# Optimization experiments

Measured on AMD Instinct MI355X. Metric: run time of the kernel, lower is better.

## Reference

```python
import jax, jax.numpy as jnp
import numpy as np

HEADS = 4
DIM_HEAD = 32
SCALE = DIM_HEAD ** -0.5


def setup_inputs() -> dict:
    key = jax.random.key(0)
    k1, k2, k3 = jax.random.split(key, 3)
    dim, hidden = 256, HEADS * DIM_HEAD
    x = jax.random.normal(k1, (4, dim, 64, 64), dtype=jnp.float32)
    w_qkv = jax.random.normal(k2, (hidden * 3, dim), dtype=jnp.float32) * (dim ** -0.5)
    w_out = jax.random.normal(k3, (dim, hidden), dtype=jnp.float32) * (hidden ** -0.5)
    b_out = jnp.zeros((dim,), dtype=jnp.float32)
    return {"x": x, "w_qkv": w_qkv, "w_out": w_out, "b_out": b_out}


def reference(x, w_qkv, w_out, b_out):
    b, c, h, w = x.shape
    # 1x1 conv (no bias) == channel matmul
    qkv = jnp.einsum('bchw,oc->bohw', x, w_qkv)           # [b, 3*hidden, h, w]
    q, k, v = jnp.split(qkv, 3, axis=1)
    def to_heads(t):
        # [b, heads*d, h, w] -> [b, heads, h*w, d]
        return t.reshape(b, HEADS, DIM_HEAD, h * w).transpose(0, 1, 3, 2)
    q, k, v = to_heads(q) * SCALE, to_heads(k), to_heads(v)
    sim = jnp.einsum('bhid,bhjd->bhij', q, k)             # [b, heads, hw, hw]
    attn = jax.nn.softmax(sim, axis=-1)
    out = jnp.einsum('bhij,bhjd->bhid', attn, v)          # [b, heads, hw, d]
    out = out.transpose(0, 1, 3, 2).reshape(b, HEADS * DIM_HEAD, h, w)
    # output 1x1 conv with bias
    return jnp.einsum('bchw,oc->bohw', out, w_out) + b_out[None, :, None, None]
```

## Files before the change

### kernel.cpp

```cpp
#include <hip/hip_runtime.h>
#include <hip/hip_fp16.h>

#define HEADS 4
#define DH    32
#define HW    4096
#define CIN   256
#define HID   128
#define KSPLIT 2
#define KHALF (HW / KSPLIT)

using half8   = __attribute__((ext_vector_type(8))) _Float16;
using half4   = __attribute__((ext_vector_type(4))) _Float16;
using half2v  = __attribute__((ext_vector_type(2))) _Float16;
using floatx4 = __attribute__((ext_vector_type(4))) float;

#define SHIFT2 4.328085122666891f
#define WQSCALE 0.25508275947f

static __device__ __forceinline__ half2v pk2(float a, float b) {
  return __builtin_bit_cast(half2v, __builtin_amdgcn_cvt_pkrtz(a, b));
}

__global__ __launch_bounds__(256) void qkv_fused(
    const float* __restrict__ w, const float* __restrict__ x,
    _Float16* __restrict__ Qw, _Float16* __restrict__ Kw,
    _Float16* __restrict__ Vtw)
{
  __shared__ float t[64][65];
  __shared__ _Float16 As[64][72];
  __shared__ _Float16 Bs[64][72];
  const int mt = blockIdx.x, nt = blockIdx.y;
  const int b = nt >> 6, p0 = (nt & 63) * 64;
  const int tid = threadIdx.x;
  const int wv = tid >> 6, lane = tid & 63, lm = lane & 15, quad = lane >> 4;
  const float wscale = (mt < 2) ? WQSCALE : 1.0f;

  const float* Ag = w + (size_t)(mt * 64) * CIN;
  const float* xb = x + (size_t)b * CIN * HW + p0;

  floatx4 acc[4] = {{0,0,0,0},{0,0,0,0},{0,0,0,0},{0,0,0,0}};

  for (int kq = 0; kq < 4; ++kq) {
    __syncthreads();
    #pragma unroll
    for (int i = 0; i < 4; ++i) {
      int ci = tid + i * 256;
      int cc = ci >> 4, p4 = (ci & 15) * 4;
      *(float4*)&t[cc][p4] =
          *(const float4*)(xb + (size_t)(kq * 64 + cc) * HW + p4);
    }
    #pragma unroll
    for (int i = 0; i < 2; ++i) {
      int ci = tid + i * 256;
      int r = ci >> 3, c8 = (ci & 7) * 8;
      const float* src = Ag + (size_t)r * CIN + kq * 64 + c8;
      float4 u0 = *(const float4*)(src);
      float4 u1 = *(const float4*)(src + 4);
      half8 h = {(_Float16)(u0.x * wscale), (_Float16)(u0.y * wscale),
                 (_Float16)(u0.z * wscale), (_Float16)(u0.w * wscale),
                 (_Float16)(u1.x * wscale), (_Float16)(u1.y * wscale),
                 (_Float16)(u1.z * wscale), (_Float16)(u1.w * wscale)};
      *(half8*)&As[r][c8] = h;
    }
    __syncthreads();
    #pragma unroll
    for (int i = 0; i < 2; ++i) {
      int idx = tid + i * 256;
      int p = idx >> 3, c0 = (idx & 7) * 8;
      half8 v;
      #pragma unroll
      for (int k = 0; k < 8; ++k) v[k] = (_Float16)t[c0 + k][p];
      *(half8*)&Bs[p][c0] = v;
    }
    __syncthreads();
    #pragma unroll
    for (int ks = 0; ks < 2; ++ks) {
      half8 a = *(const half8*)&As[wv * 16 + lm][ks * 32 + quad * 8];
      #pragma unroll
      for (int ns = 0; ns < 4; ++ns) {
        half8 bf = *(const half8*)&Bs[ns * 16 + lm][ks * 32 + quad * 8];
        acc[ns] = __builtin_amdgcn_mfma_f32_16x16x32_f16(a, bf, acc[ns], 0, 0, 0);
      }
    }
  }

  const int sec = mt >> 1;
  const int o_base = (mt & 1) * 64 + wv * 16 + quad * 4;
  const int hh = o_base >> 5, dd = o_base & 31;
  const int bh = b * HEADS + hh;
  if (sec < 2) {
    _Float16* dst = (sec == 0) ? Qw : Kw;
    #pragma unroll
    for (int ns = 0; ns < 4; ++ns) {
      int p = p0 + ns * 16 + lm;
      half4 v = {(_Float16)acc[ns][0], (_Float16)acc[ns][1],
                 (_Float16)acc[ns][2], (_Float16)acc[ns][3]};
      *(half4*)(dst + ((size_t)bh * HW + p) * DH + dd) = v;
    }
  } else {
    #pragma unroll
    for (int ns = 0; ns < 4; ++ns) {
      int p = p0 + ns * 16 + lm;
      #pragma unroll
      for (int r = 0; r < 4; ++r)
        Vtw[((size_t)bh * DH + dd + r) * HW + p] = (_Float16)acc[ns][r];
    }
  }
}

__global__ __launch_bounds__(256) void attn(
    const _Float16* __restrict__ Qw, const _Float16* __restrict__ Kw,
    const _Float16* __restrict__ Vtw, float* __restrict__ Op,
    float* __restrict__ lp)
{
  __shared__ _Float16 ks[2][64][40];
  __shared__ _Float16 vt[2][32][74];

  const int bh = blockIdx.y, qt = blockIdx.x, z = blockIdx.z;
  const int tid = threadIdx.x;
  const int wv = tid >> 6, lane = tid & 63, lm = lane & 15, quad = lane >> 4;

  const _Float16* qbase =
      Qw + ((size_t)bh * HW + qt * 128 + wv * 16 + lm) * DH + quad * 8;
  const half8 qa0 = *(const half8*)qbase;
  const half8 qa1 = *(const half8*)(qbase + (size_t)64 * DH);

  const _Float16 one = (_Float16)1.0f;
  const half4 ones4 = {one, one, one, one};
  const floatx4 shiftc = {-SHIFT2, -SHIFT2, -SHIFT2, -SHIFT2};

  floatx4 oT[2][2] = {{{0,0,0,0},{0,0,0,0}},{{0,0,0,0},{0,0,0,0}}};
  floatx4 l4[2]    = {{0,0,0,0},{0,0,0,0}};

  const _Float16* kbase = Kw  + (size_t)bh * HW * DH + (size_t)z * KHALF * DH;
  const _Float16* vbase = Vtw + (size_t)bh * DH * HW + (size_t)z * KHALF;
  const int kr = tid >> 2, kc = (tid & 3) * 8;
  const int vr = tid >> 3, vc = (tid & 7) * 8;

  half8 kA = *(const half8*)(kbase + (size_t)kr * DH + kc);
  half8 vA = *(const half8*)(vbase + (size_t)vr * HW + vc);
  *(half8*)&ks[0][kr][kc] = kA;
  *(half8*)&vt[0][vr][vc] = vA;
  kA = *(const half8*)(kbase + ((size_t)64 + kr) * DH + kc);
  vA = *(const half8*)(vbase + (size_t)vr * HW + 64 + vc);
  __syncthreads();

  for (int it = 0; it < KHALF / 64; ++it) {
    const int ph = it & 1, nx = ph ^ 1;

    half8 kf[4];
    half4 vf[4][2];
    #pragma unroll
    for (int f = 0; f < 4; ++f) {
      kf[f]    = *(const half8*)&ks[ph][f * 16 + lm][quad * 8];
      vf[f][0] = *(const half4*)&vt[ph][lm][f * 16 + quad * 4];
      vf[f][1] = *(const half4*)&vt[ph][16 + lm][f * 16 + quad * 4];
    }

    *(half8*)&ks[nx][kr][kc] = kA;
    *(half8*)&vt[nx][vr][vc] = vA;
    size_t koff = (size_t)(it + 2) * 64;
    if (koff > KHALF - 64) koff = KHALF - 64;
    kA = *(const half8*)(kbase + (koff + kr) * DH + kc);
    vA = *(const half8*)(vbase + (size_t)vr * HW + koff + vc);

    #pragma unroll
    for (int f = 0; f < 4; ++f) {
      floatx4 sT0 = __builtin_amdgcn_mfma_f32_16x16x32_f16(kf[f], qa0, shiftc, 0, 0, 0);
      floatx4 sT1 = __builtin_amdgcn_mfma_f32_16x16x32_f16(kf[f], qa1, shiftc, 0, 0, 0);
      half2v a0 = pk2(__builtin_amdgcn_exp2f(sT0[0]), __builtin_amdgcn_exp2f(sT0[1]));
      half2v b0 = pk2(__builtin_amdgcn_exp2f(sT0[2]), __builtin_amdgcn_exp2f(sT0[3]));
      half2v a1 = pk2(__builtin_amdgcn_exp2f(sT1[0]), __builtin_amdgcn_exp2f(sT1[1]));
      half2v b1 = pk2(__builtin_amdgcn_exp2f(sT1[2]), __builtin_amdgcn_exp2f(sT1[3]));
      half4 pb0 = {a0.x, a0.y, b0.x, b0.y};
      half4 pb1 = {a1.x, a1.y, b1.x, b1.y};
      l4[0] = __builtin_amdgcn_mfma_f32_16x16x16f16(ones4, pb0, l4[0], 0, 0, 0);
      l4[1] = __builtin_amdgcn_mfma_f32_16x16x16f16(ones4, pb1, l4[1], 0, 0, 0);
      #pragma unroll
      for (int g = 0; g < 2; ++g) {
        oT[0][g] = __builtin_amdgcn_mfma_f32_16x16x16f16(vf[f][g], pb0, oT[0][g], 0, 0, 0);
        oT[1][g] = __builtin_amdgcn_mfma_f32_16x16x16f16(vf[f][g], pb1, oT[1][g], 0, 0, 0);
      }
    }
    __syncthreads();
  }

  const int b = bh >> 2, hh = bh & 3;
  #pragma unroll
  for (int t = 0; t < 2; ++t) {
    const int row = qt * 128 + t * 64 + wv * 16 + lm;
    float* obase = Op +
        ((size_t)z * 4 * HW + (size_t)b * HW + row) * HID + hh * DH;
    #pragma unroll
    for (int g = 0; g < 2; ++g) {
      float4 v = {oT[t][g][0], oT[t][g][1], oT[t][g][2], oT[t][g][3]};
      *(float4*)(obase + g * 16 + quad * 4) = v;
    }
    if (quad == 0)
      lp[(size_t)z * HEADS * 4 * HW + (size_t)bh * HW + row] = l4[t][0];
  }
}

__global__ __launch_bounds__(256) void out_gemm(
    const float* __restrict__ wo, const float* __restrict__ Op,
    const float* __restrict__ lp, const float* __restrict__ bo,
    float* __restrict__ out)
{
  __shared__ _Float16 As[64][136];
  __shared__ _Float16 Bs[64][136];
  __shared__ float os[64][68];
  __shared__ float inv_l[64][4];
  const int mt = blockIdx.x, nt = blockIdx.y;
  const int b = nt >> 6, p0 = (nt & 63) * 64;
  const int tid = threadIdx.x;
  const int wv = tid >> 6, lane = tid & 63, lm = lane & 15, quad = lane >> 4;

  {
    const int p = tid >> 2, hh = tid & 3;
    const size_t qi = (size_t)(b * HEADS + hh) * HW + p0 + p;
    inv_l[p][hh] = 1.0f / (lp[qi] + lp[(size_t)HEADS * 4 * HW + qi]);
  }
  __syncthreads();

  const float* Ag  = wo + (size_t)(mt * 64) * HID;
  const float* Bp0 = Op + ((size_t)b * HW + p0) * HID;
  const float* Bp1 = Bp0 + (size_t)4 * HW * HID;

  #pragma unroll
  for (int i = 0; i < 4; ++i) {
    int ci = tid + i * 256;
    int r = ci >> 4, c8 = (ci & 15) * 8;
    const float* src = Ag + (size_t)r * HID + c8;
    float4 u0 = *(const float4*)(src);
    float4 u1 = *(const float4*)(src + 4);
    half8 h = {(_Float16)u0.x, (_Float16)u0.y, (_Float16)u0.z, (_Float16)u0.w,
               (_Float16)u1.x, (_Float16)u1.y, (_Float16)u1.z, (_Float16)u1.w};
    *(half8*)&As[r][c8] = h;

    const float* s0 = Bp0 + (size_t)r * HID + c8;
    const float* s1 = Bp1 + (size_t)r * HID + c8;
    float4 o0 = *(const float4*)(s0);
    float4 o1 = *(const float4*)(s0 + 4);
    float4 o2 = *(const float4*)(s1);
    float4 o3 = *(const float4*)(s1 + 4);
    const float sc = inv_l[r][c8 >> 5];
    half8 hb = {(_Float16)((o0.x + o2.x) * sc), (_Float16)((o0.y + o2.y) * sc),
                (_Float16)((o0.z + o2.z) * sc), (_Float16)((o0.w + o2.w) * sc),
                (_Float16)((o1.x + o3.x) * sc), (_Float16)((o1.y + o3.y) * sc),
                (_Float16)((o1.z + o3.z) * sc), (_Float16)((o1.w + o3.w) * sc)};
    *(half8*)&Bs[r][c8] = hb;
  }
  __syncthreads();

  floatx4 acc[4] = {{0,0,0,0},{0,0,0,0},{0,0,0,0},{0,0,0,0}};
  #pragma unroll
  for (int ks = 0; ks < 4; ++ks) {
    half8 a = *(const half8*)&As[wv * 16 + lm][ks * 32 + quad * 8];
    #pragma unroll
    for (int ns = 0; ns < 4; ++ns) {
      half8 bf = *(const half8*)&Bs[ns * 16 + lm][ks * 32 + quad * 8];
      acc[ns] = __builtin_amdgcn_mfma_f32_16x16x32_f16(a, bf, acc[ns], 0, 0, 0);
    }
  }

  #pragma unroll
  for (int ns = 0; ns < 4; ++ns)
    #pragma unroll
    for (int r = 0; r < 4; ++r)
      os[wv * 16 + quad * 4 + r][ns * 16 + lm] = acc[ns][r];
  __syncthreads();

  const int o = tid >> 2, pq = (tid & 3) * 16;
  const float bias = bo[mt * 64 + o];
  float* dst = out + ((size_t)(b * CIN + mt * 64 + o)) * HW + p0 + pq;
  #pragma unroll
  for (int j = 0; j < 4; ++j) {
    float4 v = *(const float4*)&os[o][pq + j * 4];
    v.x += bias; v.y += bias; v.z += bias; v.w += bias;
    *(float4*)(dst + j * 4) = v;
  }
}

extern "C" void kernel_launch(void* const* d_in, const int* in_sizes, int n_in,
                              void* d_out, int out_size, void* d_ws, size_t ws_size,
                              hipStream_t stream)
{
  const float* x     = (const float*)d_in[0];
  const float* w_qkv = (const float*)d_in[1];
  const float* w_out = (const float*)d_in[2];
  const float* b_out = (const float*)d_in[3];
  float* out = (float*)d_out;

  char* ws = (char*)d_ws;
  _Float16* Qw  = (_Float16*)(ws);
  _Float16* Kw  = (_Float16*)(ws + (4u  << 20));
  _Float16* Vtw = (_Float16*)(ws + (8u  << 20));
  float*    Op  = (float*)   (ws + (12u << 20));
  float*    lp  = (float*)   (ws + (28u << 20));

  dim3 blk(256);
  qkv_fused<<<dim3(6, 256), blk, 0, stream>>>(w_qkv, x, Qw, Kw, Vtw);
  attn<<<dim3(32, 16, KSPLIT), blk, 0, stream>>>(Qw, Kw, Vtw, Op, lp);
  out_gemm<<<dim3(4, 256), blk, 0, stream>>>(w_out, Op, lp, b_out, out);
}
```

Before: 163.5 us.

## Load K/V fragments directly from global into registers and remap blocks for L2 locality

Removes the LDS staging and per-iteration __syncthreads in the attention kernel: each wave now loads its K and V MFMA fragments straight from global memory into registers, double-buffered across iterations. The grid is flattened to 1D with a swizzle that groups blocks sharing the same (bh, z) K/V slice, presumably so they land on the same XCD/L2. The trade-off is that each of the four waves fetches the full K/V tile redundantly, with narrow strided loads (especially for V), and it relies on cache hits instead of shared memory reuse.

New measurement: 264.5 us. +61.8%, slower.

```diff
diff --git a/kernel.cpp b/kernel.cpp
--- a/kernel.cpp
+++ b/kernel.cpp
@@ -8,6 +8,7 @@
 #define HID   128
 #define KSPLIT 2
 #define KHALF (HW / KSPLIT)
+#define NIT   (KHALF / 64)
 
 using half8   = __attribute__((ext_vector_type(8))) _Float16;
 using half4   = __attribute__((ext_vector_type(4))) _Float16;
@@ -113,10 +114,11 @@
     const _Float16* __restrict__ Vtw, float* __restrict__ Op,
     float* __restrict__ lp)
 {
-  __shared__ _Float16 ks[2][64][40];
-  __shared__ _Float16 vt[2][32][74];
-
-  const int bh = blockIdx.y, qt = blockIdx.x, z = blockIdx.z;
+  const int id = blockIdx.x;
+  const int combo = (id & 7) * 4 + ((id >> 3) >> 5);
+  const int qt = (id >> 3) & 31;
+  const int bh = combo >> 1, z = combo & 1;
+
   const int tid = threadIdx.x;
   const int wv = tid >> 6, lane = tid & 63, lm = lane & 15, quad = lane >> 4;
 
@@ -132,58 +134,66 @@
   floatx4 oT[2][2] = {{{0,0,0,0},{0,0,0,0}},{{0,0,0,0},{0,0,0,0}}};
   floatx4 l4[2]    = {{0,0,0,0},{0,0,0,0}};
 
-  const _Float16* kbase = Kw  + (size_t)bh * HW * DH + (size_t)z * KHALF * DH;
-  const _Float16* vbase = Vtw + (size_t)bh * DH * HW + (size_t)z * KHALF;
-  const int kr = tid >> 2, kc = (tid & 3) * 8;
-  const int vr = tid >> 3, vc = (tid & 7) * 8;
-
-  half8 kA = *(const half8*)(kbase + (size_t)kr * DH + kc);
-  half8 vA = *(const half8*)(vbase + (size_t)vr * HW + vc);
-  *(half8*)&ks[0][kr][kc] = kA;
-  *(half8*)&vt[0][vr][vc] = vA;
-  kA = *(const half8*)(kbase + ((size_t)64 + kr) * DH + kc);
-  vA = *(const half8*)(vbase + (size_t)vr * HW + 64 + vc);
-  __syncthreads();
-
-  for (int it = 0; it < KHALF / 64; ++it) {
-    const int ph = it & 1, nx = ph ^ 1;
-
-    half8 kf[4];
-    half4 vf[4][2];
-    #pragma unroll
-    for (int f = 0; f < 4; ++f) {
-      kf[f]    = *(const half8*)&ks[ph][f * 16 + lm][quad * 8];
-      vf[f][0] = *(const half4*)&vt[ph][lm][f * 16 + quad * 4];
-      vf[f][1] = *(const half4*)&vt[ph][16 + lm][f * 16 + quad * 4];
-    }
-
-    *(half8*)&ks[nx][kr][kc] = kA;
-    *(half8*)&vt[nx][vr][vc] = vA;
-    size_t koff = (size_t)(it + 2) * 64;
-    if (koff > KHALF - 64) koff = KHALF - 64;
-    kA = *(const half8*)(kbase + (koff + kr) * DH + kc);
-    vA = *(const half8*)(vbase + (size_t)vr * HW + koff + vc);
-
-    #pragma unroll
-    for (int f = 0; f < 4; ++f) {
-      floatx4 sT0 = __builtin_amdgcn_mfma_f32_16x16x32_f16(kf[f], qa0, shiftc, 0, 0, 0);
-      floatx4 sT1 = __builtin_amdgcn_mfma_f32_16x16x32_f16(kf[f], qa1, shiftc, 0, 0, 0);
-      half2v a0 = pk2(__builtin_amdgcn_exp2f(sT0[0]), __builtin_amdgcn_exp2f(sT0[1]));
-      half2v b0 = pk2(__builtin_amdgcn_exp2f(sT0[2]), __builtin_amdgcn_exp2f(sT0[3]));
-      half2v a1 = pk2(__builtin_amdgcn_exp2f(sT1[0]), __builtin_amdgcn_exp2f(sT1[1]));
-      half2v b1 = pk2(__builtin_amdgcn_exp2f(sT1[2]), __builtin_amdgcn_exp2f(sT1[3]));
-      half4 pb0 = {a0.x, a0.y, b0.x, b0.y};
-      half4 pb1 = {a1.x, a1.y, b1.x, b1.y};
-      l4[0] = __builtin_amdgcn_mfma_f32_16x16x16f16(ones4, pb0, l4[0], 0, 0, 0);
-      l4[1] = __builtin_amdgcn_mfma_f32_16x16x16f16(ones4, pb1, l4[1], 0, 0, 0);
-      #pragma unroll
-      for (int g = 0; g < 2; ++g) {
-        oT[0][g] = __builtin_amdgcn_mfma_f32_16x16x16f16(vf[f][g], pb0, oT[0][g], 0, 0, 0);
-        oT[1][g] = __builtin_amdgcn_mfma_f32_16x16x16f16(vf[f][g], pb1, oT[1][g], 0, 0, 0);
-      }
-    }
-    __syncthreads();
-  }
+  const _Float16* kp  = Kw  + (size_t)bh * HW * DH + (size_t)z * KHALF * DH
+                        + (size_t)lm * DH + quad * 8;
+  const _Float16* vp0 = Vtw + (size_t)bh * DH * HW + (size_t)z * KHALF
+                        + (size_t)lm * HW + quad * 4;
+  const _Float16* vp1 = vp0 + (size_t)16 * HW;
+
+  half8 kf0[4], kf1[4];
+  half4 vf0[4][2], vf1[4][2];
+
+#define LOADKV(KF, VF, itv)                                                  \
+  {                                                                          \
+    const _Float16* kp_  = kp  + (size_t)(itv) * 64 * DH;                    \
+    const _Float16* vp0_ = vp0 + (size_t)(itv) * 64;                         \
+    const _Float16* vp1_ = vp1 + (size_t)(itv) * 64;                         \
+    KF[0] = *(const half8*)(kp_);                                            \
+    KF[1] = *(const half8*)(kp_ + 16 * DH);                                  \
+    KF[2] = *(const half8*)(kp_ + 32 * DH);                                  \
+    KF[3] = *(const half8*)(kp_ + 48 * DH);                                  \
+    VF[0][0] = *(const half4*)(vp0_);                                        \
+    VF[0][1] = *(const half4*)(vp1_);                                        \
+    VF[1][0] = *(const half4*)(vp0_ + 16);                                   \
+    VF[1][1] = *(const half4*)(vp1_ + 16);                                   \
+    VF[2][0] = *(const half4*)(vp0_ + 32);                                   \
+    VF[2][1] = *(const half4*)(vp1_ + 32);                                   \
+    VF[3][0] = *(const half4*)(vp0_ + 48);                                   \
+    VF[3][1] = *(const half4*)(vp1_ + 48);                                   \
+  }
+
+#define COMPUTE(KF, VF)                                                      \
+  {                                                                          \
+    _Pragma("unroll")                                                        \
+    for (int f = 0; f < 4; ++f) {                                            \
+      floatx4 sT0 = __builtin_amdgcn_mfma_f32_16x16x32_f16(KF[f], qa0, shiftc, 0, 0, 0); \
+      floatx4 sT1 = __builtin_amdgcn_mfma_f32_16x16x32_f16(KF[f], qa1, shiftc, 0, 0, 0); \
+      half2v a0 = pk2(__builtin_amdgcn_exp2f(sT0[0]), __builtin_amdgcn_exp2f(sT0[1])); \
+      half2v b0 = pk2(__builtin_amdgcn_exp2f(sT0[2]), __builtin_amdgcn_exp2f(sT0[3])); \
+      half2v a1 = pk2(__builtin_amdgcn_exp2f(sT1[0]), __builtin_amdgcn_exp2f(sT1[1])); \
+      half2v b1 = pk2(__builtin_amdgcn_exp2f(sT1[2]), __builtin_amdgcn_exp2f(sT1[3])); \
+      half4 pb0 = {a0.x, a0.y, b0.x, b0.y};                                  \
+      half4 pb1 = {a1.x, a1.y, b1.x, b1.y};                                  \
+      l4[0] = __builtin_amdgcn_mfma_f32_16x16x16f16(ones4, pb0, l4[0], 0, 0, 0); \
+      l4[1] = __builtin_amdgcn_mfma_f32_16x16x16f16(ones4, pb1, l4[1], 0, 0, 0); \
+      _Pragma("unroll")                                                      \
+      for (int g = 0; g < 2; ++g) {                                          \
+        oT[0][g] = __builtin_amdgcn_mfma_f32_16x16x16f16(VF[f][g], pb0, oT[0][g], 0, 0, 0); \
+        oT[1][g] = __builtin_amdgcn_mfma_f32_16x16x16f16(VF[f][g], pb1, oT[1][g], 0, 0, 0); \
+      }                                                                      \
+    }                                                                        \
+  }
+
+  LOADKV(kf0, vf0, 0);
+  for (int it = 0; it < NIT; it += 2) {
+    LOADKV(kf1, vf1, it + 1);
+    COMPUTE(kf0, vf0);
+    const int i2 = (it + 2 < NIT) ? it + 2 : NIT - 1;
+    LOADKV(kf0, vf0, i2);
+    COMPUTE(kf1, vf1);
+  }
+#undef LOADKV
+#undef COMPUTE
 
   const int b = bh >> 2, hh = bh & 3;
   #pragma unroll
@@ -300,6 +310,6 @@
 
   dim3 blk(256);
   qkv_fused<<<dim3(6, 256), blk, 0, stream>>>(w_qkv, x, Qw, Kw, Vtw);
-  attn<<<dim3(32, 16, KSPLIT), blk, 0, stream>>>(Qw, Kw, Vtw, Op, lp);
+  attn<<<dim3(1024), blk, 0, stream>>>(Qw, Kw, Vtw, Op, lp);
   out_gemm<<<dim3(4, 256), blk, 0, stream>>>(w_out, Op, lp, b_out, out);
 }
```

## Switch attention kernel to 32x32x16 MFMA with permlane swap and swizzled LDS

Applied to the files above, without the earlier changes.

Restructures the attention inner loop from 16x16 MFMA tiles to 32x32x16 MFMA tiles. Each wave now owns 32 query rows, and P is repacked in registers via v_permlane32_swap so it can feed the PV MFMA directly. The row sum is now computed with scalar adds plus a cross-half shuffle instead of a ones-matrix MFMA. K/V shared-memory tiles use an XOR swizzle with unpadded V rows to avoid bank conflicts. The goal is fewer MFMA issues and less LDS traffic per FLOP, at the cost of extra VALU adds and more register pressure.

Result: no change. 161.8 us (-1.0%).

```diff
diff --git a/kernel.cpp b/kernel.cpp
--- a/kernel.cpp
+++ b/kernel.cpp
@@ -8,17 +8,20 @@
 #define HID   128
 #define KSPLIT 2
 #define KHALF (HW / KSPLIT)
-
-using half8   = __attribute__((ext_vector_type(8))) _Float16;
-using half4   = __attribute__((ext_vector_type(4))) _Float16;
-using half2v  = __attribute__((ext_vector_type(2))) _Float16;
-using floatx4 = __attribute__((ext_vector_type(4))) float;
+#define NIT   (KHALF / 64)
+
+using half8    = __attribute__((ext_vector_type(8))) _Float16;
+using half4    = __attribute__((ext_vector_type(4))) _Float16;
+using half2v   = __attribute__((ext_vector_type(2))) _Float16;
+using floatx4  = __attribute__((ext_vector_type(4))) float;
+using floatx16 = __attribute__((ext_vector_type(16))) float;
+using uint4v   = __attribute__((ext_vector_type(4))) unsigned;
 
 #define SHIFT2 4.328085122666891f
 #define WQSCALE 0.25508275947f
 
-static __device__ __forceinline__ half2v pk2(float a, float b) {
-  return __builtin_bit_cast(half2v, __builtin_amdgcn_cvt_pkrtz(a, b));
+static __device__ __forceinline__ unsigned pkr(float a, float b) {
+  return __builtin_bit_cast(unsigned, __builtin_amdgcn_cvt_pkrtz(a, b));
 }
 
 __global__ __launch_bounds__(256) void qkv_fused(
@@ -114,91 +117,99 @@
     float* __restrict__ lp)
 {
   __shared__ _Float16 ks[2][64][40];
-  __shared__ _Float16 vt[2][32][74];
+  __shared__ _Float16 vt[2][32][72];
 
   const int bh = blockIdx.y, qt = blockIdx.x, z = blockIdx.z;
   const int tid = threadIdx.x;
-  const int wv = tid >> 6, lane = tid & 63, lm = lane & 15, quad = lane >> 4;
+  const int wv = tid >> 6, lane = tid & 63;
+  const int l31 = lane & 31, hi = lane >> 5;
 
   const _Float16* qbase =
-      Qw + ((size_t)bh * HW + qt * 128 + wv * 16 + lm) * DH + quad * 8;
-  const half8 qa0 = *(const half8*)qbase;
-  const half8 qa1 = *(const half8*)(qbase + (size_t)64 * DH);
-
-  const _Float16 one = (_Float16)1.0f;
-  const half4 ones4 = {one, one, one, one};
-  const floatx4 shiftc = {-SHIFT2, -SHIFT2, -SHIFT2, -SHIFT2};
-
-  floatx4 oT[2][2] = {{{0,0,0,0},{0,0,0,0}},{{0,0,0,0},{0,0,0,0}}};
-  floatx4 l4[2]    = {{0,0,0,0},{0,0,0,0}};
+      Qw + ((size_t)bh * HW + qt * 128 + wv * 32 + l31) * DH + hi * 8;
+  const half8 qb0 = *(const half8*)qbase;
+  const half8 qb1 = *(const half8*)(qbase + 16);
+
+  const floatx16 shift16 = {-SHIFT2,-SHIFT2,-SHIFT2,-SHIFT2,
+                            -SHIFT2,-SHIFT2,-SHIFT2,-SHIFT2,
+                            -SHIFT2,-SHIFT2,-SHIFT2,-SHIFT2,
+                            -SHIFT2,-SHIFT2,-SHIFT2,-SHIFT2};
+  floatx16 oT = {0,0,0,0,0,0,0,0,0,0,0,0,0,0,0,0};
+  float lsum = 0.0f;
 
   const _Float16* kbase = Kw  + (size_t)bh * HW * DH + (size_t)z * KHALF * DH;
   const _Float16* vbase = Vtw + (size_t)bh * DH * HW + (size_t)z * KHALF;
   const int kr = tid >> 2, kc = (tid & 3) * 8;
   const int vr = tid >> 3, vc = (tid & 7) * 8;
+  const int kwc = (((tid & 3) ^ ((kr >> 3) & 3)) << 3);
+  const int vwc = (((tid & 7) ^ ((vr >> 3) & 3)) << 3);
+  const int kx = (l31 >> 3) & 3;
 
   half8 kA = *(const half8*)(kbase + (size_t)kr * DH + kc);
   half8 vA = *(const half8*)(vbase + (size_t)vr * HW + vc);
-  *(half8*)&ks[0][kr][kc] = kA;
-  *(half8*)&vt[0][vr][vc] = vA;
+  *(half8*)&ks[0][kr][kwc] = kA;
+  *(half8*)&vt[0][vr][vwc] = vA;
   kA = *(const half8*)(kbase + ((size_t)64 + kr) * DH + kc);
   vA = *(const half8*)(vbase + (size_t)vr * HW + 64 + vc);
   __syncthreads();
 
-  for (int it = 0; it < KHALF / 64; ++it) {
+  for (int it = 0; it < NIT; ++it) {
     const int ph = it & 1, nx = ph ^ 1;
 
-    half8 kf[4];
-    half4 vf[4][2];
-    #pragma unroll
-    for (int f = 0; f < 4; ++f) {
-      kf[f]    = *(const half8*)&ks[ph][f * 16 + lm][quad * 8];
-      vf[f][0] = *(const half4*)&vt[ph][lm][f * 16 + quad * 4];
-      vf[f][1] = *(const half4*)&vt[ph][16 + lm][f * 16 + quad * 4];
-    }
-
-    *(half8*)&ks[nx][kr][kc] = kA;
-    *(half8*)&vt[nx][vr][vc] = vA;
+    half8 ka[2][2];
+    half8 va[4];
+    #pragma unroll
+    for (int t = 0; t < 2; ++t)
+      #pragma unroll
+      for (int d = 0; d < 2; ++d)
+        ka[t][d] = *(const half8*)&ks[ph][t * 32 + l31][((d * 2 + hi) ^ kx) << 3];
+    #pragma unroll
+    for (int k4 = 0; k4 < 4; ++k4)
+      va[k4] = *(const half8*)&vt[ph][l31][((k4 * 2 + hi) ^ kx) << 3];
+
+    *(half8*)&ks[nx][kr][kwc] = kA;
+    *(half8*)&vt[nx][vr][vwc] = vA;
     size_t koff = (size_t)(it + 2) * 64;
     if (koff > KHALF - 64) koff = KHALF - 64;
     kA = *(const half8*)(kbase + (koff + kr) * DH + kc);
     vA = *(const half8*)(vbase + (size_t)vr * HW + koff + vc);
 
     #pragma unroll
-    for (int f = 0; f < 4; ++f) {
-      floatx4 sT0 = __builtin_amdgcn_mfma_f32_16x16x32_f16(kf[f], qa0, shiftc, 0, 0, 0);
-      floatx4 sT1 = __builtin_amdgcn_mfma_f32_16x16x32_f16(kf[f], qa1, shiftc, 0, 0, 0);
-      half2v a0 = pk2(__builtin_amdgcn_exp2f(sT0[0]), __builtin_amdgcn_exp2f(sT0[1]));
-      half2v b0 = pk2(__builtin_amdgcn_exp2f(sT0[2]), __builtin_amdgcn_exp2f(sT0[3]));
-      half2v a1 = pk2(__builtin_amdgcn_exp2f(sT1[0]), __builtin_amdgcn_exp2f(sT1[1]));
-      half2v b1 = pk2(__builtin_amdgcn_exp2f(sT1[2]), __builtin_amdgcn_exp2f(sT1[3]));
-      half4 pb0 = {a0.x, a0.y, b0.x, b0.y};
-      half4 pb1 = {a1.x, a1.y, b1.x, b1.y};
-      l4[0] = __builtin_amdgcn_mfma_f32_16x16x16f16(ones4, pb0, l4[0], 0, 0, 0);
-      l4[1] = __builtin_amdgcn_mfma_f32_16x16x16f16(ones4, pb1, l4[1], 0, 0, 0);
-      #pragma unroll
-      for (int g = 0; g < 2; ++g) {
-        oT[0][g] = __builtin_amdgcn_mfma_f32_16x16x16f16(vf[f][g], pb0, oT[0][g], 0, 0, 0);
-        oT[1][g] = __builtin_amdgcn_mfma_f32_16x16x16f16(vf[f][g], pb1, oT[1][g], 0, 0, 0);
-      }
+    for (int t = 0; t < 2; ++t) {
+      floatx16 sT = __builtin_amdgcn_mfma_f32_32x32x16_f16(ka[t][0], qb0, shift16, 0, 0, 0);
+      sT = __builtin_amdgcn_mfma_f32_32x32x16_f16(ka[t][1], qb1, sT, 0, 0, 0);
+      float e[16];
+      #pragma unroll
+      for (int r = 0; r < 16; ++r) e[r] = __builtin_amdgcn_exp2f(sT[r]);
+      lsum += (((e[0]+e[1])+(e[2]+e[3]))+((e[4]+e[5])+(e[6]+e[7])))
+            + (((e[8]+e[9])+(e[10]+e[11]))+((e[12]+e[13])+(e[14]+e[15])));
+      unsigned w0 = pkr(e[0],  e[1]),  w1 = pkr(e[2],  e[3]);
+      unsigned w2 = pkr(e[4],  e[5]),  w3 = pkr(e[6],  e[7]);
+      unsigned w4 = pkr(e[8],  e[9]),  w5 = pkr(e[10], e[11]);
+      unsigned w6 = pkr(e[12], e[13]), w7 = pkr(e[14], e[15]);
+      asm("v_permlane32_swap_b32 %0, %1" : "+v"(w0), "+v"(w2));
+      asm("v_permlane32_swap_b32 %0, %1" : "+v"(w1), "+v"(w3));
+      asm("v_permlane32_swap_b32 %0, %1" : "+v"(w4), "+v"(w6));
+      asm("v_permlane32_swap_b32 %0, %1" : "+v"(w5), "+v"(w7));
+      uint4v lo4 = {w0, w1, w2, w3}, hi4 = {w4, w5, w6, w7};
+      half8 pbLo = __builtin_bit_cast(half8, lo4);
+      half8 pbHi = __builtin_bit_cast(half8, hi4);
+      oT = __builtin_amdgcn_mfma_f32_32x32x16_f16(va[2*t],     pbLo, oT, 0, 0, 0);
+      oT = __builtin_amdgcn_mfma_f32_32x32x16_f16(va[2*t + 1], pbHi, oT, 0, 0, 0);
     }
     __syncthreads();
   }
 
+  lsum += __shfl_xor(lsum, 32, 64);
   const int b = bh >> 2, hh = bh & 3;
-  #pragma unroll
-  for (int t = 0; t < 2; ++t) {
-    const int row = qt * 128 + t * 64 + wv * 16 + lm;
-    float* obase = Op +
-        ((size_t)z * 4 * HW + (size_t)b * HW + row) * HID + hh * DH;
-    #pragma unroll
-    for (int g = 0; g < 2; ++g) {
-      float4 v = {oT[t][g][0], oT[t][g][1], oT[t][g][2], oT[t][g][3]};
-      *(float4*)(obase + g * 16 + quad * 4) = v;
-    }
-    if (quad == 0)
-      lp[(size_t)z * HEADS * 4 * HW + (size_t)bh * HW + row] = l4[t][0];
-  }
+  const int row = qt * 128 + wv * 32 + l31;
+  float* obase = Op + ((size_t)z * 4 * HW + (size_t)b * HW + row) * HID + hh * DH;
+  #pragma unroll
+  for (int r0 = 0; r0 < 4; ++r0) {
+    float4 v = {oT[4*r0], oT[4*r0+1], oT[4*r0+2], oT[4*r0+3]};
+    *(float4*)(obase + 8 * r0 + 4 * hi) = v;
+  }
+  if (lane < 32)
+    lp[(size_t)z * HEADS * 4 * HW + (size_t)bh * HW + row] = lsum;
 }
 
 __global__ __launch_bounds__(256) void out_gemm(
```
